# Kernel tuning notes

Hardware: AMD Instinct MI355X
Metric: run time of the kernel (lower is better)

Reference implementation:

```python
import jax, jax.numpy as jnp
import numpy as np

B, T, C, H = 2, 2048, 1024, 16
D = C // H  # head dim 64

def setup_inputs() -> dict:
    key = jax.random.key(0)
    k1, k2, k3 = jax.random.split(key, 3)
    x = jax.random.normal(k1, (B, T, C), dtype=jnp.float32)
    W_attn = jax.random.normal(k2, (C, 3 * C), dtype=jnp.float32) * (1.0 / np.sqrt(C))
    b_attn = jnp.zeros((3 * C,), dtype=jnp.float32)
    W_proj = jax.random.normal(k3, (C, C), dtype=jnp.float32) * (1.0 / np.sqrt(C))
    b_proj = jnp.zeros((C,), dtype=jnp.float32)
    return {"x": x, "W_attn": W_attn, "b_attn": b_attn, "W_proj": W_proj, "b_proj": b_proj}

def reference(x, W_attn, b_attn, W_proj, b_proj):
    Bsz, Tlen, Cdim = x.shape
    qkv = x @ W_attn + b_attn  # [B,T,3C]
    q, k, v = jnp.split(qkv, 3, axis=2)
    # [B,T,C] -> [B,H,T,D]
    q = q.reshape(Bsz, Tlen, H, D).transpose(0, 2, 1, 3)
    k = k.reshape(Bsz, Tlen, H, D).transpose(0, 2, 1, 3)
    v = v.reshape(Bsz, Tlen, H, D).transpose(0, 2, 1, 3)
    att = jnp.einsum('bhqd,bhkd->bhqk', q, k) * (1.0 / np.sqrt(D))
    causal = jnp.tril(jnp.ones((Tlen, Tlen), dtype=bool))
    att = jnp.where(causal[None, None, :, :], att, jnp.float32(-jnp.inf))
    att = jax.nn.softmax(att, axis=-1)
    y = jnp.einsum('bhqk,bhkd->bhqd', att, v)  # [B,H,T,D]
    y = y.transpose(0, 2, 1, 3).reshape(Bsz, Tlen, Cdim)
    return y @ W_proj + b_proj
```

## Files before the change

kernel.cpp:

```cpp
#include <hip/hip_runtime.h>
#include <math.h>

#define BSZ 2
#define TSEQ 2048
#define CDIM 1024
#define HNUM 16

typedef __attribute__((ext_vector_type(8))) short bhalf8;
typedef __attribute__((ext_vector_type(4))) short bhalf4;
typedef __attribute__((ext_vector_type(4))) float floatx4;

__device__ __forceinline__ unsigned short f2bf(float f) {
    union { float f; unsigned u; } v;
    v.f = f;
    unsigned r = v.u + 0x7FFFu + ((v.u >> 16) & 1u);
    return (unsigned short)(r >> 16);
}

__device__ __forceinline__ floatx4 fx4_zero() { floatx4 z = {0.f,0.f,0.f,0.f}; return z; }

typedef __attribute__((address_space(3))) unsigned int lds_u32;
typedef const __attribute__((address_space(1))) unsigned int g_u32;
__device__ __forceinline__ void async_copy16(const void* g, void* l) {
    __builtin_amdgcn_global_load_lds((g_u32*)g, (lds_u32*)l, 16, 0, 0);
}

__device__ __forceinline__ void trans_tile(
    const float* __restrict__ W, unsigned short* __restrict__ Wt,
    int K, int N, int n0, int k0, int tid, float (*t)[33])
{
    const int tx = tid & 31, ty = tid >> 5;
#pragma unroll
    for (int i = 0; i < 4; ++i)
        t[ty + i * 8][tx] = W[(size_t)(k0 + ty + i * 8) * N + n0 + tx];
    __syncthreads();
#pragma unroll
    for (int i = 0; i < 4; ++i)
        Wt[(size_t)(n0 + ty + i * 8) * K + k0 + tx] = f2bf(t[tx][ty + i * 8]);
}

__global__ __launch_bounds__(256) void prepass(
    const float* __restrict__ x, unsigned short* __restrict__ xb,
    const float* __restrict__ Wa, unsigned short* __restrict__ WtA,
    const float* __restrict__ Wp, unsigned short* __restrict__ WtP)
{
    __shared__ float t[32][33];
    const int bid = blockIdx.x;
    const int tid = threadIdx.x;
    if (bid < 2048) {
        size_t i = ((size_t)bid * 256 + tid) * 8;
        float4 a = *(const float4*)(x + i);
        float4 b = *(const float4*)(x + i + 4);
        uint4 o;
        o.x = (unsigned)f2bf(a.x) | ((unsigned)f2bf(a.y) << 16);
        o.y = (unsigned)f2bf(a.z) | ((unsigned)f2bf(a.w) << 16);
        o.z = (unsigned)f2bf(b.x) | ((unsigned)f2bf(b.y) << 16);
        o.w = (unsigned)f2bf(b.z) | ((unsigned)f2bf(b.w) << 16);
        *(uint4*)(xb + i) = o;
    } else if (bid < 5120) {
        int tl = bid - 2048;
        trans_tile(Wa, WtA, 1024, 3072, (tl % 96) * 32, (tl / 96) * 32, tid, t);
    } else {
        int tl = bid - 5120;
        trans_tile(Wp, WtP, 1024, 1024, (tl % 32) * 32, (tl / 32) * 32, tid, t);
    }
}

template<int BM, int BN, bool OUT_BF16>
__global__ __launch_bounds__(256) void gemm_bt(
    const unsigned short* __restrict__ A, const unsigned short* __restrict__ Bt,
    const float* __restrict__ bias, void* __restrict__ Cp,
    int M, int N, int K, int v_start, unsigned short* __restrict__ vt, int q_end)
{
    constexpr int ALINES = BM / 64;
    constexpr int BLINES = BN / 64;
    constexpr int MT = BM / 32;
    constexpr int NT = BN / 32;
    __shared__ unsigned short As[2][BM * 32];
    __shared__ unsigned short Bs[2][BN * 32];

    const int tid   = threadIdx.x;
    const int bm    = blockIdx.y;
    const int bn    = blockIdx.x;
    const int wave  = tid >> 6;
    const int col16 = tid & 15;
    const int quad  = (tid & 63) >> 4;
    const int wm    = (wave >> 1) * (BM / 2);
    const int wn    = (wave & 1) * (BN / 2);

    floatx4 acc[MT][NT];
#pragma unroll
    for (int i = 0; i < MT; ++i)
#pragma unroll
        for (int j = 0; j < NT; ++j) acc[i][j] = fx4_zero();

    const int gr = tid >> 2;
    const int gk = (((tid & 3) + 4 - ((tid >> 3) & 3)) & 3) * 8;
    const unsigned short* Ab = A  + (size_t)(bm * BM + gr) * K + gk;
    const unsigned short* Bb = Bt + (size_t)(bn * BN + gr) * K + gk;

    const int sw8 = ((quad + (col16 >> 1)) & 3) * 8;

#define STAGE(k0, bf) { \
    char* AsB = (char*)As[bf] + wave * 1024; \
    char* BsB = (char*)Bs[bf] + wave * 1024; \
    _Pragma("unroll") \
    for (int l = 0; l < ALINES; ++l) \
        async_copy16(Ab + (size_t)l * 64 * K + (k0), AsB + l * 4096); \
    _Pragma("unroll") \
    for (int l = 0; l < BLINES; ++l) \
        async_copy16(Bb + (size_t)l * 64 * K + (k0), BsB + l * 4096); }

#define COMPUTE(bf) { \
    bhalf8 a[MT], b[NT]; \
    _Pragma("unroll") \
    for (int i = 0; i < MT; ++i) \
        a[i] = *(const bhalf8*)&As[bf][(wm + i * 16 + col16) * 32 + sw8]; \
    _Pragma("unroll") \
    for (int j = 0; j < NT; ++j) \
        b[j] = *(const bhalf8*)&Bs[bf][(wn + j * 16 + col16) * 32 + sw8]; \
    _Pragma("unroll") \
    for (int i = 0; i < MT; ++i) \
        _Pragma("unroll") \
        for (int j = 0; j < NT; ++j) \
            acc[i][j] = __builtin_amdgcn_mfma_f32_16x16x32_bf16(a[i], b[j], acc[i][j], 0, 0, 0); }

    STAGE(0, 0);
    __syncthreads();
    int buf = 0;
    for (int k0 = 0; k0 < K - 32; k0 += 32) {
        STAGE(k0 + 32, buf ^ 1);
        COMPUTE(buf);
        __syncthreads();
        buf ^= 1;
    }
    COMPUTE(buf);
#undef STAGE
#undef COMPUTE

    const int colbase = bn * BN + wn;
    const bool vpath = (v_start >= 0) && (colbase >= v_start);
    const float csc = (colbase < q_end) ? 0.18033688f : 1.0f;
#pragma unroll
    for (int j = 0; j < NT; ++j) {
        int col = colbase + j * 16 + col16;
        float bv = bias[col];
#pragma unroll
        for (int i = 0; i < MT; ++i) {
            if (vpath) {
                int row0 = bm * BM + wm + i * 16 + quad * 4;
                ushort4 o;
                o.x = f2bf((acc[i][j][0] + bv) * csc);
                o.y = f2bf((acc[i][j][1] + bv) * csc);
                o.z = f2bf((acc[i][j][2] + bv) * csc);
                o.w = f2bf((acc[i][j][3] + bv) * csc);
                size_t vrow = (size_t)((row0 >> 11) * 1024 + (col - v_start));
                *(ushort4*)(vt + vrow * 2048 + (row0 & 2047)) = o;
            } else {
#pragma unroll
                for (int r = 0; r < 4; ++r) {
                    int row = bm * BM + wm + i * 16 + quad * 4 + r;
                    float v = (acc[i][j][r] + bv) * csc;
                    if (OUT_BF16)
                        ((unsigned short*)Cp)[(size_t)row * N + col] = f2bf(v);
                    else
                        ((float*)Cp)[(size_t)row * N + col] = v;
                }
            }
        }
    }
}

template<bool DIAG>
__device__ __forceinline__ void attn_tile(
    const unsigned short* __restrict__ Ks, const unsigned short* __restrict__ Vt,
    const bhalf8* qf, floatx4* oT, floatx4& accl,
    int col16, int quad, int qloc)
{
    const int sx = col16 & 7;
    const floatx4 minusC = {-17.31234049f, -17.31234049f, -17.31234049f, -17.31234049f};
    const bhalf4 ones = {0x3F80, 0x3F80, 0x3F80, 0x3F80};

    floatx4 s[4];
#pragma unroll
    for (int n = 0; n < 4; ++n) {
        const int row = 16 * n + col16;
        bhalf8 k0 = *(const bhalf8*)&Ks[row * 64 + ((quad ^ sx) * 8)];
        bhalf8 k1 = *(const bhalf8*)&Ks[row * 64 + (((4 + quad) ^ sx) * 8)];
        floatx4 t = __builtin_amdgcn_mfma_f32_16x16x32_bf16(k0, qf[0], minusC, 0, 0, 0);
        s[n] = __builtin_amdgcn_mfma_f32_16x16x32_bf16(k1, qf[1], t, 0, 0, 0);
    }

    bhalf4 pb[4];
#pragma unroll
    for (int n = 0; n < 4; ++n) {
        unsigned a[4];
#pragma unroll
        for (int r = 0; r < 4; ++r) {
            float p = exp2f(s[n][r]);
            if (DIAG) {
                if (16 * n + quad * 4 + r > qloc) p = 0.f;
            }
            a[r] = __float_as_uint(p) + 0x8000u;
        }
        union { unsigned u[2]; bhalf4 b; } uu;
        uu.u[0] = (a[0] >> 16) | (a[1] & 0xffff0000u);
        uu.u[1] = (a[2] >> 16) | (a[3] & 0xffff0000u);
        pb[n] = uu.b;
        accl = __builtin_amdgcn_mfma_f32_16x16x16bf16_1k(ones, pb[n], accl, 0, 0, 0);
    }

#pragma unroll
    for (int n = 0; n < 4; ++n) {
#pragma unroll
        for (int dt = 0; dt < 4; ++dt) {
            const int d = 16 * dt + col16;
            const bhalf4 av = *(const bhalf4*)&Vt[d * 76 + 16 * n + quad * 4];
            oT[dt] = __builtin_amdgcn_mfma_f32_16x16x16bf16_1k(av, pb[n], oT[dt], 0, 0, 0);
        }
    }
}

__global__ __launch_bounds__(256) void attn_mfma(
    const unsigned short* __restrict__ qkv,
    const unsigned short* __restrict__ vT,
    unsigned short* __restrict__ yout)
{
    __shared__ unsigned short Kbuf[2][64 * 64];
    __shared__ unsigned short Vbuf[2][64 * 76];

    const int tid   = threadIdx.x;
    const int wave  = tid >> 6;
    const int col16 = tid & 15;
    const int quad  = (tid & 63) >> 4;
    const int qb    = (int)gridDim.y - 1 - (int)blockIdx.y;
    const int bh    = blockIdx.x;
    const int b     = bh >> 4;
    const int h     = bh & 15;

    const unsigned short* base  = qkv + (size_t)b * TSEQ * 3072 + h * 64;
    const unsigned short* kbase = base + CDIM;
    const unsigned short* vtb   = vT + (size_t)(b * 1024 + h * 64) * 2048;

    bhalf8 qf[2];
    {
        const unsigned short* qrow =
            base + (size_t)(qb * 64 + wave * 16 + col16) * 3072 + quad * 8;
        qf[0] = *(const bhalf8*)qrow;
        qf[1] = *(const bhalf8*)(qrow + 32);
    }

    const int krow = tid >> 3;
    const int kchk = (tid & 7) ^ (krow & 7);
    const unsigned short* ksrc0 = kbase + (size_t)krow * 3072 + kchk * 8;
    const unsigned short* ksrc1 = kbase + (size_t)(krow + 32) * 3072 + kchk * 8;

    const int vd  = tid >> 3;
    const int vt0 = (tid & 7) * 8;
    const unsigned short* vsrc0 = vtb + (size_t)vd * 2048 + vt0;
    const unsigned short* vsrc1 = vtb + (size_t)(vd + 32) * 2048 + vt0;

#define KSTAGE(kb, bf) { \
    char* Kd = (char*)Kbuf[bf] + wave * 1024; \
    async_copy16(ksrc0 + (size_t)(kb) * 64 * 3072, Kd); \
    async_copy16(ksrc1 + (size_t)(kb) * 64 * 3072, Kd + 4096); }

    floatx4 oT[4];
#pragma unroll
    for (int dt = 0; dt < 4; ++dt) oT[dt] = fx4_zero();
    floatx4 accl = fx4_zero();
    const int qloc = wave * 16 + col16;

    {
        uint4 nv0 = *(const uint4*)vsrc0;
        uint4 nv1 = *(const uint4*)vsrc1;
        KSTAGE(0, 0);
        *(uint4*)&Vbuf[0][vd * 76 + vt0]        = nv0;
        *(uint4*)&Vbuf[0][(vd + 32) * 76 + vt0] = nv1;
    }
    __syncthreads();
    int buf = 0;
    for (int kb = 0; kb < qb; ++kb) {
        uint4 nv0 = *(const uint4*)(vsrc0 + (size_t)(kb + 1) * 64);
        uint4 nv1 = *(const uint4*)(vsrc1 + (size_t)(kb + 1) * 64);
        KSTAGE(kb + 1, buf ^ 1);
        attn_tile<false>(Kbuf[buf], Vbuf[buf], qf, oT, accl, col16, quad, qloc);
        *(uint4*)&Vbuf[buf ^ 1][vd * 76 + vt0]        = nv0;
        *(uint4*)&Vbuf[buf ^ 1][(vd + 32) * 76 + vt0] = nv1;
        __syncthreads();
        buf ^= 1;
    }
    attn_tile<true>(Kbuf[buf], Vbuf[buf], qf, oT, accl, col16, quad, qloc);
#undef KSTAGE

    const float inv = 1.0f / accl[0];
    const size_t row = (size_t)b * TSEQ + (size_t)qb * 64 + wave * 16 + col16;
#pragma unroll
    for (int dt = 0; dt < 4; ++dt) {
        ushort4 o;
        o.x = f2bf(oT[dt][0] * inv);
        o.y = f2bf(oT[dt][1] * inv);
        o.z = f2bf(oT[dt][2] * inv);
        o.w = f2bf(oT[dt][3] * inv);
        *(ushort4*)(yout + row * CDIM + h * 64 + 16 * dt + quad * 4) = o;
    }
}

extern "C" void kernel_launch(void* const* d_in, const int* in_sizes, int n_in,
                              void* d_out, int out_size, void* d_ws, size_t ws_size,
                              hipStream_t stream)
{
    const float* x      = (const float*)d_in[0];
    const float* W_attn = (const float*)d_in[1];
    const float* b_attn = (const float*)d_in[2];
    const float* W_proj = (const float*)d_in[3];
    const float* b_proj = (const float*)d_in[4];
    float* out = (float*)d_out;

    unsigned short* qkv = (unsigned short*)d_ws;
    unsigned short* y   = qkv + (size_t)4096 * 3072;
    unsigned short* xb  = y   + (size_t)4096 * 1024;
    unsigned short* WtA = xb  + (size_t)4096 * 1024;
    unsigned short* WtP = WtA + (size_t)3072 * 1024;
    unsigned short* vT  = WtP + (size_t)1024 * 1024;

    prepass<<<dim3(6144), 256, 0, stream>>>(x, xb, W_attn, WtA, W_proj, WtP);

    gemm_bt<128, 128, true><<<dim3(3072 / 128, 4096 / 128), 256, 0, stream>>>(
        xb, WtA, b_attn, qkv, 4096, 3072, 1024, 2048, vT, 1024);

    attn_mfma<<<dim3(BSZ * HNUM, TSEQ / 64), 256, 0, stream>>>(qkv, vT, y);

    gemm_bt<64, 64, false><<<dim3(1024 / 64, 4096 / 64), 256, 0, stream>>>(
        y, WtP, b_proj, out, 4096, 1024, 1024, -1, nullptr, 0);
}
```

Baseline: 181.0 us.

## Use 128-row query blocks with 8 waves sharing K/V tiles in attention

The attention kernel now processes 128 query rows per block with 512 threads, so each staged 64-key K/V tile is reused by twice as many waves, halving global/LDS staging per query. Each thread now loads a single 16-byte chunk of K and V per stage. The padded V layout (stride 76) is replaced with an XOR-swizzled 64-wide layout to avoid bank conflicts without padding. Per-wave diagonal handling is added, so the first four waves do masked work on the last-but-one tile and then sit idle on the final tile, and coarser blocks reduce grid-level parallelism and causal load balance.

```diff
diff --git a/kernel.cpp b/kernel.cpp
--- a/kernel.cpp
+++ b/kernel.cpp
@@ -178,6 +178,7 @@
     int col16, int quad, int qloc)
 {
     const int sx = col16 & 7;
+    const int qh = quad >> 1, ql = (quad & 1) * 4;
     const floatx4 minusC = {-17.31234049f, -17.31234049f, -17.31234049f, -17.31234049f};
     const bhalf4 ones = {0x3F80, 0x3F80, 0x3F80, 0x3F80};
 
@@ -214,20 +215,20 @@
     for (int n = 0; n < 4; ++n) {
 #pragma unroll
         for (int dt = 0; dt < 4; ++dt) {
-            const int d = 16 * dt + col16;
-            const bhalf4 av = *(const bhalf4*)&Vt[d * 76 + 16 * n + quad * 4];
+            const int idx = (16 * dt + col16) * 64 + (((2 * n + qh) ^ sx) << 3) + ql;
+            const bhalf4 av = *(const bhalf4*)&Vt[idx];
             oT[dt] = __builtin_amdgcn_mfma_f32_16x16x16bf16_1k(av, pb[n], oT[dt], 0, 0, 0);
         }
     }
 }
 
-__global__ __launch_bounds__(256) void attn_mfma(
+__global__ __launch_bounds__(512) void attn_mfma(
     const unsigned short* __restrict__ qkv,
     const unsigned short* __restrict__ vT,
     unsigned short* __restrict__ yout)
 {
     __shared__ unsigned short Kbuf[2][64 * 64];
-    __shared__ unsigned short Vbuf[2][64 * 76];
+    __shared__ unsigned short Vbuf[2][64 * 64];
 
     const int tid   = threadIdx.x;
     const int wave  = tid >> 6;
@@ -245,56 +246,55 @@
     bhalf8 qf[2];
     {
         const unsigned short* qrow =
-            base + (size_t)(qb * 64 + wave * 16 + col16) * 3072 + quad * 8;
+            base + (size_t)(qb * 128 + wave * 16 + col16) * 3072 + quad * 8;
         qf[0] = *(const bhalf8*)qrow;
         qf[1] = *(const bhalf8*)(qrow + 32);
     }
 
     const int krow = tid >> 3;
     const int kchk = (tid & 7) ^ (krow & 7);
-    const unsigned short* ksrc0 = kbase + (size_t)krow * 3072 + kchk * 8;
-    const unsigned short* ksrc1 = kbase + (size_t)(krow + 32) * 3072 + kchk * 8;
+    const unsigned short* ksrc = kbase + (size_t)krow * 3072 + kchk * 8;
 
     const int vd  = tid >> 3;
     const int vt0 = (tid & 7) * 8;
-    const unsigned short* vsrc0 = vtb + (size_t)vd * 2048 + vt0;
-    const unsigned short* vsrc1 = vtb + (size_t)(vd + 32) * 2048 + vt0;
-
-#define KSTAGE(kb, bf) { \
-    char* Kd = (char*)Kbuf[bf] + wave * 1024; \
-    async_copy16(ksrc0 + (size_t)(kb) * 64 * 3072, Kd); \
-    async_copy16(ksrc1 + (size_t)(kb) * 64 * 3072, Kd + 4096); }
+    const int vsl = vd * 64 + (((tid & 7) ^ (vd & 7)) * 8);
+    const unsigned short* vsrc = vtb + (size_t)vd * 2048 + vt0;
+
+#define KSTAGE(kb, bf) \
+    async_copy16(ksrc + (size_t)(kb) * 64 * 3072, (char*)Kbuf[bf] + wave * 1024);
 
     floatx4 oT[4];
 #pragma unroll
     for (int dt = 0; dt < 4; ++dt) oT[dt] = fx4_zero();
     floatx4 accl = fx4_zero();
-    const int qloc = wave * 16 + col16;
+    const int qloc  = (wave & 3) * 16 + col16;
+    const int wdiag = 2 * qb + (wave >> 2);
 
     {
-        uint4 nv0 = *(const uint4*)vsrc0;
-        uint4 nv1 = *(const uint4*)vsrc1;
+        uint4 nv = *(const uint4*)vsrc;
         KSTAGE(0, 0);
-        *(uint4*)&Vbuf[0][vd * 76 + vt0]        = nv0;
-        *(uint4*)&Vbuf[0][(vd + 32) * 76 + vt0] = nv1;
+        *(uint4*)&Vbuf[0][vsl] = nv;
     }
     __syncthreads();
     int buf = 0;
-    for (int kb = 0; kb < qb; ++kb) {
-        uint4 nv0 = *(const uint4*)(vsrc0 + (size_t)(kb + 1) * 64);
-        uint4 nv1 = *(const uint4*)(vsrc1 + (size_t)(kb + 1) * 64);
+    const int last = 2 * qb + 1;
+    for (int kb = 0; kb < last; ++kb) {
+        uint4 nv = *(const uint4*)(vsrc + (size_t)(kb + 1) * 64);
         KSTAGE(kb + 1, buf ^ 1);
-        attn_tile<false>(Kbuf[buf], Vbuf[buf], qf, oT, accl, col16, quad, qloc);
-        *(uint4*)&Vbuf[buf ^ 1][vd * 76 + vt0]        = nv0;
-        *(uint4*)&Vbuf[buf ^ 1][(vd + 32) * 76 + vt0] = nv1;
+        if (kb < wdiag)
+            attn_tile<false>(Kbuf[buf], Vbuf[buf], qf, oT, accl, col16, quad, qloc);
+        else
+            attn_tile<true>(Kbuf[buf], Vbuf[buf], qf, oT, accl, col16, quad, qloc);
+        *(uint4*)&Vbuf[buf ^ 1][vsl] = nv;
         __syncthreads();
         buf ^= 1;
     }
-    attn_tile<true>(Kbuf[buf], Vbuf[buf], qf, oT, accl, col16, quad, qloc);
+    if (wdiag == last)
+        attn_tile<true>(Kbuf[buf], Vbuf[buf], qf, oT, accl, col16, quad, qloc);
 #undef KSTAGE
 
     const float inv = 1.0f / accl[0];
-    const size_t row = (size_t)b * TSEQ + (size_t)qb * 64 + wave * 16 + col16;
+    const size_t row = (size_t)b * TSEQ + (size_t)qb * 128 + wave * 16 + col16;
 #pragma unroll
     for (int dt = 0; dt < 4; ++dt) {
         ushort4 o;
@@ -329,7 +329,7 @@
     gemm_bt<128, 128, true><<<dim3(3072 / 128, 4096 / 128), 256, 0, stream>>>(
         xb, WtA, b_attn, qkv, 4096, 3072, 1024, 2048, vT, 1024);
 
-    attn_mfma<<<dim3(BSZ * HNUM, TSEQ / 64), 256, 0, stream>>>(qkv, vT, y);
+    attn_mfma<<<dim3(BSZ * HNUM, TSEQ / 128), 512, 0, stream>>>(qkv, vT, y);
 
     gemm_bt<64, 64, false><<<dim3(1024 / 64, 4096 / 64), 256, 0, stream>>>(
         y, WtP, b_proj, out, 4096, 1024, 1024, -1, nullptr, 0);
```

After: 192.1 us. 1.06x slower.
